# Kernel tuning notes

Hardware: AMD Instinct MI355X
Metric: run time of the kernel (lower is better)

Reference implementation:

```python
import jax, jax.numpy as jnp
import numpy as np

TAU = 1.0   # ltc_params['tau_constant']
DT = 0.1    # LTCCell default dt
UNFOLDS = 6 # ltc_params['ode_unfolds']
B, S, D, H, O = 512, 512, 128, 128, 1


def setup_inputs() -> dict:
    key = jax.random.key(0)
    ks = jax.random.split(key, 7)
    sc = lambda n: 1.0 / np.sqrt(n)
    return {
        "x":    jax.random.normal(ks[0], (B, S, D), dtype=jnp.float32),
        "W_in": jax.random.normal(ks[1], (H, D), dtype=jnp.float32) * sc(D),
        "b_in": jax.random.normal(ks[2], (H,), dtype=jnp.float32) * sc(D),
        "W_r":  jax.random.normal(ks[3], (H, H), dtype=jnp.float32) * sc(H),
        "b_r":  jax.random.normal(ks[4], (H,), dtype=jnp.float32) * sc(H),
        "W_fc": jax.random.normal(ks[5], (O, H), dtype=jnp.float32) * sc(H),
        "b_fc": jax.random.normal(ks[6], (O,), dtype=jnp.float32) * sc(H),
    }


def reference(x, W_in, b_in, W_r, b_r, W_fc, b_fc):
    # input_map(x[:, t]) is invariant across the inner unfold loop -> precompute once.
    xin_all = jnp.einsum('bsd,hd->bsh', x, W_in) + b_in  # [B,S,H]

    def step(h, xin):  # h: [B,H], xin: [B,H]
        for _ in range(UNFOLDS):  # small fixed count, unrolled
            v = jnp.tanh(xin + h @ W_r.T + b_r)
            h = h + DT * (-h / TAU + v)
        return h, None

    h0 = jnp.zeros((x.shape[0], W_r.shape[0]), dtype=x.dtype)
    h, _ = jax.lax.scan(step, h0, jnp.swapaxes(xin_all, 0, 1))  # scan over seq
    return (h @ W_fc.T + b_fc).squeeze(-1)  # [B]
```

## Files before the change

### kernel.cpp

```cpp
#include <hip/hip_runtime.h>


typedef _Float16 v2h __attribute__((ext_vector_type(2)));

#define S_LEN 512
#define HDIM 128
#define BATCH 512
#define NUNF 6
#define DTC 0.1f

__device__ __forceinline__ v2h pk2h(float a, float b) {
    return __builtin_bit_cast(v2h, __builtin_amdgcn_cvt_pkrtz(a, b));
}

__device__ __forceinline__ float fast_tanh(float y) {
    float u = __expf(2.0f * y);
    return 1.0f - __fdividef(2.0f, u + 1.0f);
}

__global__ __launch_bounds__(256, 2)
void xin_kernel(const float* __restrict__ x,
                const float* __restrict__ W_in,
                const float* __restrict__ b_in,
                unsigned int* __restrict__ xin)
{
    __shared__ __align__(16) _Float16 xt[128 * HDIM];
    const int tid  = threadIdx.x;
    const int w    = tid >> 6;
    const int lane = tid & 63;
    const int bs0  = blockIdx.x * 128;

    const float4* xg = reinterpret_cast<const float4*>(x + (size_t)bs0 * HDIM);
#pragma unroll
    for (int i = 0; i < 16; ++i) {
        int idx = i * 1024 + tid * 4;
        float4 v = xg[idx >> 2];
        v2h* d = reinterpret_cast<v2h*>(xt + idx);
        d[0] = pk2h(v.x, v.y);
        d[1] = pk2h(v.z, v.w);
    }

    v2h wi0[64], wi1[64];
    {
        const float4* r0 = reinterpret_cast<const float4*>(W_in + (size_t)lane * HDIM);
        const float4* r1 = reinterpret_cast<const float4*>(W_in + (size_t)(lane + 64) * HDIM);
#pragma unroll
        for (int j = 0; j < 32; ++j) {
            float4 f = r0[j];
            wi0[2*j]   = pk2h(f.x, f.y);
            wi0[2*j+1] = pk2h(f.z, f.w);
            float4 g = r1[j];
            wi1[2*j]   = pk2h(g.x, g.y);
            wi1[2*j+1] = pk2h(g.z, g.w);
        }
    }
    const float bi0 = b_in[lane], bi1 = b_in[lane + 64];
    __syncthreads();

    for (int rr = 0; rr < 32; ++rr) {
        const int r = w * 32 + rr;
        const float4* hp = reinterpret_cast<const float4*>(xt + r * HDIM);
        float a0 = 0.f, a1 = 0.f, c0 = 0.f, c1 = 0.f;
#pragma unroll
        for (int j = 0; j < 16; ++j) {
            float4 q = hp[j];
            const v2h* hh = reinterpret_cast<const v2h*>(&q);
            a0 = __builtin_amdgcn_fdot2(wi0[4*j+0], hh[0], a0, false);
            a1 = __builtin_amdgcn_fdot2(wi0[4*j+1], hh[1], a1, false);
            a0 = __builtin_amdgcn_fdot2(wi0[4*j+2], hh[2], a0, false);
            a1 = __builtin_amdgcn_fdot2(wi0[4*j+3], hh[3], a1, false);
            c0 = __builtin_amdgcn_fdot2(wi1[4*j+0], hh[0], c0, false);
            c1 = __builtin_amdgcn_fdot2(wi1[4*j+1], hh[1], c1, false);
            c0 = __builtin_amdgcn_fdot2(wi1[4*j+2], hh[2], c0, false);
            c1 = __builtin_amdgcn_fdot2(wi1[4*j+3], hh[3], c1, false);
        }
        v2h pk = pk2h(a0 + a1 + bi0, c0 + c1 + bi1);
        xin[(size_t)(bs0 + r) * 64 + lane] = __builtin_bit_cast(unsigned int, pk);
    }
}

__global__ __launch_bounds__(64, 1)
void ltc_kernel(const unsigned int* __restrict__ xin,
                const float* __restrict__ W_r,
                const float* __restrict__ b_r,
                const float* __restrict__ W_fc,
                const float* __restrict__ b_fc,
                float* __restrict__ out)
{
    const int b  = blockIdx.x;
    const int ln = threadIdx.x;
    const int o0 = ln, o1 = ln + 64;

    __shared__ __align__(16) v2h hbuf[64];

    v2h wr0[64], wr1[64];
    {
        const float4* lo0 = reinterpret_cast<const float4*>(W_r + (size_t)o0 * HDIM);
        const float4* hi0 = reinterpret_cast<const float4*>(W_r + (size_t)o0 * HDIM + 64);
        const float4* lo1 = reinterpret_cast<const float4*>(W_r + (size_t)o1 * HDIM);
        const float4* hi1 = reinterpret_cast<const float4*>(W_r + (size_t)o1 * HDIM + 64);
#pragma unroll
        for (int j = 0; j < 16; ++j) {
            float4 a = lo0[j], h = hi0[j];
            wr0[4*j+0] = pk2h(a.x, h.x);
            wr0[4*j+1] = pk2h(a.y, h.y);
            wr0[4*j+2] = pk2h(a.z, h.z);
            wr0[4*j+3] = pk2h(a.w, h.w);
            float4 c = lo1[j], d = hi1[j];
            wr1[4*j+0] = pk2h(c.x, d.x);
            wr1[4*j+1] = pk2h(c.y, d.y);
            wr1[4*j+2] = pk2h(c.z, d.z);
            wr1[4*j+3] = pk2h(c.w, d.w);
        }
    }
    const float br0 = b_r[o0], br1 = b_r[o1];
    const unsigned int* xrow = xin + (size_t)b * S_LEN * 64;

    float h0 = 0.f, h1 = 0.f;
    hbuf[ln] = v2h{(_Float16)0.f, (_Float16)0.f};
    unsigned int xcur = xrow[ln];

    for (int s = 0; s < S_LEN; ++s) {
        unsigned int xnext = 0;
        if (s + 1 < S_LEN) xnext = xrow[(s + 1) * 64 + ln];
        v2h xp = __builtin_bit_cast(v2h, xcur);
        const float xs0 = (float)xp.x + br0;
        const float xs1 = (float)xp.y + br1;

#pragma unroll
        for (int u = 0; u < NUNF; ++u) {
            const float4* hp = reinterpret_cast<const float4*>(hbuf);
            float a0 = 0.f, a1 = 0.f, c0 = 0.f, c1 = 0.f;
#pragma unroll
            for (int j = 0; j < 16; ++j) {
                float4 q = hp[j];
                const v2h* hh = reinterpret_cast<const v2h*>(&q);
                a0 = __builtin_amdgcn_fdot2(wr0[4*j+0], hh[0], a0, false);
                a1 = __builtin_amdgcn_fdot2(wr0[4*j+1], hh[1], a1, false);
                a0 = __builtin_amdgcn_fdot2(wr0[4*j+2], hh[2], a0, false);
                a1 = __builtin_amdgcn_fdot2(wr0[4*j+3], hh[3], a1, false);
                c0 = __builtin_amdgcn_fdot2(wr1[4*j+0], hh[0], c0, false);
                c1 = __builtin_amdgcn_fdot2(wr1[4*j+1], hh[1], c1, false);
                c0 = __builtin_amdgcn_fdot2(wr1[4*j+2], hh[2], c0, false);
                c1 = __builtin_amdgcn_fdot2(wr1[4*j+3], hh[3], c1, false);
            }
            float v0 = fast_tanh(xs0 + a0 + a1);
            float v1 = fast_tanh(xs1 + c0 + c1);
            h0 = h0 + DTC * (v0 - h0);
            h1 = h1 + DTC * (v1 - h1);
            hbuf[ln] = pk2h(h0, h1);
        }
        xcur = xnext;
    }

    float partial = h0 * W_fc[o0] + h1 * W_fc[o1];
#pragma unroll
    for (int d = 1; d < 64; d <<= 1) partial += __shfl_xor(partial, d);
    if (ln == 0) out[b] = partial + b_fc[0];
}

__global__ __launch_bounds__(256, 2)
void ltc_fallback(const float* __restrict__ x,
                  const float* __restrict__ W_in,
                  const float* __restrict__ b_in,
                  const float* __restrict__ W_r,
                  const float* __restrict__ b_r,
                  const float* __restrict__ W_fc,
                  const float* __restrict__ b_fc,
                  float* __restrict__ out)
{
    const int b     = blockIdx.x;
    const int tid   = threadIdx.x;
    const int o     = tid >> 1;
    const int kh    = tid & 1;
    const int kbase = kh * 64;

    __shared__ __align__(16) _Float16 hbuf[2][HDIM];
    __shared__ __align__(16) _Float16 xbuf[2][HDIM];
    __shared__ float red[4];

    v2h wr[32], wi[32];
    {
        const float4* wrp = reinterpret_cast<const float4*>(W_r  + o * HDIM + kbase);
        const float4* wip = reinterpret_cast<const float4*>(W_in + o * HDIM + kbase);
#pragma unroll
        for (int j = 0; j < 16; ++j) {
            float4 f = wrp[j];
            wr[2*j]   = pk2h(f.x, f.y);
            wr[2*j+1] = pk2h(f.z, f.w);
            float4 g = wip[j];
            wi[2*j]   = pk2h(g.x, g.y);
            wi[2*j+1] = pk2h(g.z, g.w);
        }
    }
    const float binv = b_in[o];
    const float brv  = b_r[o];
    const float* x_row = x + (size_t)b * S_LEN * HDIM;
    float h_o = 0.0f;

    if (tid < HDIM) {
        xbuf[0][tid] = (_Float16)x_row[tid];
        hbuf[0][tid] = (_Float16)0.0f;
    }
    __syncthreads();

    for (int s = 0; s < S_LEN; ++s) {
        float xnext = 0.0f;
        if (tid < HDIM && s + 1 < S_LEN)
            xnext = x_row[(size_t)(s + 1) * HDIM + tid];

        float xin_o;
        {
            const float4* hp = reinterpret_cast<const float4*>(&xbuf[s & 1][kbase]);
            float4 hv[8];
#pragma unroll
            for (int j = 0; j < 8; ++j) hv[j] = hp[j];
            const v2h* hh = reinterpret_cast<const v2h*>(hv);
            float a0 = 0.f, a1 = 0.f, a2 = 0.f, a3 = 0.f;
#pragma unroll
            for (int j = 0; j < 32; j += 4) {
                a0 = __builtin_amdgcn_fdot2(wi[j],   hh[j],   a0, false);
                a1 = __builtin_amdgcn_fdot2(wi[j+1], hh[j+1], a1, false);
                a2 = __builtin_amdgcn_fdot2(wi[j+2], hh[j+2], a2, false);
                a3 = __builtin_amdgcn_fdot2(wi[j+3], hh[j+3], a3, false);
            }
            float sum = (a0 + a1) + (a2 + a3);
            sum += __shfl_xor(sum, 1);
            xin_o = sum + binv;
        }

#pragma unroll
        for (int u = 0; u < NUNF; ++u) {
            const float4* hp = reinterpret_cast<const float4*>(&hbuf[u & 1][kbase]);
            float4 hv[8];
#pragma unroll
            for (int j = 0; j < 8; ++j) hv[j] = hp[j];
            const v2h* hh = reinterpret_cast<const v2h*>(hv);
            float a0 = 0.f, a1 = 0.f, a2 = 0.f, a3 = 0.f;
#pragma unroll
            for (int j = 0; j < 32; j += 4) {
                a0 = __builtin_amdgcn_fdot2(wr[j],   hh[j],   a0, false);
                a1 = __builtin_amdgcn_fdot2(wr[j+1], hh[j+1], a1, false);
                a2 = __builtin_amdgcn_fdot2(wr[j+2], hh[j+2], a2, false);
                a3 = __builtin_amdgcn_fdot2(wr[j+3], hh[j+3], a3, false);
            }
            float sum = (a0 + a1) + (a2 + a3);
            sum += __shfl_xor(sum, 1);
            float yv = xin_o + brv + sum;
            float v  = fast_tanh(yv);
            h_o = h_o + DTC * (v - h_o);
            if ((tid & 1) == 0)
                hbuf[(u + 1) & 1][o] = (_Float16)h_o;
            if (u == NUNF - 1 && tid < HDIM && s + 1 < S_LEN)
                xbuf[(s + 1) & 1][tid] = (_Float16)xnext;
            __syncthreads();
        }
    }

    float partial = 0.0f;
    if ((tid & 1) == 0) partial = h_o * W_fc[o];
#pragma unroll
    for (int d = 1; d < 64; d <<= 1) partial += __shfl_xor(partial, d);
    if ((tid & 63) == 0) red[tid >> 6] = partial;
    __syncthreads();
    if (tid == 0) out[b] = red[0] + red[1] + red[2] + red[3] + b_fc[0];
}

extern "C" void kernel_launch(void* const* d_in, const int* in_sizes, int n_in,
                              void* d_out, int out_size, void* d_ws, size_t ws_size,
                              hipStream_t stream) {
    const float* x    = (const float*)d_in[0];
    const float* W_in = (const float*)d_in[1];
    const float* b_in = (const float*)d_in[2];
    const float* W_r  = (const float*)d_in[3];
    const float* b_r  = (const float*)d_in[4];
    const float* W_fc = (const float*)d_in[5];
    const float* b_fc = (const float*)d_in[6];
    float* outp = (float*)d_out;
    (void)in_sizes; (void)n_in; (void)out_size;

    const size_t need = (size_t)BATCH * S_LEN * 64 * sizeof(unsigned int);
    if (ws_size >= need) {
        unsigned int* xin = (unsigned int*)d_ws;
        xin_kernel<<<dim3(2048), dim3(256), 0, stream>>>(x, W_in, b_in, xin);
        ltc_kernel<<<dim3(512), dim3(64), 0, stream>>>(xin, W_r, b_r, W_fc, b_fc, outp);
    } else {
        ltc_fallback<<<dim3(512), dim3(256), 0, stream>>>(x, W_in, b_in, W_r, b_r, W_fc, b_fc, outp);
    }
}
```

Before: 1.620 ms.

## Split recurrent step across two wavefronts, one output neuron per thread

Moves the recurrent kernel from one 64-lane wavefront handling two hidden units per lane to a 128-thread block where each thread owns one hidden unit. This halves the per-thread dot-product chain and the register-held weights. In exchange it needs a block-wide barrier after every unfold, uses double-buffered shared hidden state, and adds a cross-wave reduction at the end. The serial recurrence is latency-bound, so the gain depends on whether the shorter dependency chain outweighs the barrier cost.

```diff
diff --git a/kernel.cpp b/kernel.cpp
--- a/kernel.cpp
+++ b/kernel.cpp
@@ -79,7 +79,7 @@
     }
 }
 
-__global__ __launch_bounds__(64, 1)
+__global__ __launch_bounds__(128, 1)
 void ltc_kernel(const unsigned int* __restrict__ xin,
                 const float* __restrict__ W_r,
                 const float* __restrict__ b_r,
@@ -87,76 +87,66 @@
                 const float* __restrict__ b_fc,
                 float* __restrict__ out)
 {
-    const int b  = blockIdx.x;
-    const int ln = threadIdx.x;
-    const int o0 = ln, o1 = ln + 64;
-
-    __shared__ __align__(16) v2h hbuf[64];
-
-    v2h wr0[64], wr1[64];
+    const int b   = blockIdx.x;
+    const int tid = threadIdx.x;
+    const int w   = tid >> 6;
+    const int ln  = tid & 63;
+    const int od  = tid;
+
+    __shared__ __align__(16) _Float16 hbuf[2][HDIM];
+    __shared__ float red[2];
+
+    v2h wr[64];
     {
-        const float4* lo0 = reinterpret_cast<const float4*>(W_r + (size_t)o0 * HDIM);
-        const float4* hi0 = reinterpret_cast<const float4*>(W_r + (size_t)o0 * HDIM + 64);
-        const float4* lo1 = reinterpret_cast<const float4*>(W_r + (size_t)o1 * HDIM);
-        const float4* hi1 = reinterpret_cast<const float4*>(W_r + (size_t)o1 * HDIM + 64);
-#pragma unroll
-        for (int j = 0; j < 16; ++j) {
-            float4 a = lo0[j], h = hi0[j];
-            wr0[4*j+0] = pk2h(a.x, h.x);
-            wr0[4*j+1] = pk2h(a.y, h.y);
-            wr0[4*j+2] = pk2h(a.z, h.z);
-            wr0[4*j+3] = pk2h(a.w, h.w);
-            float4 c = lo1[j], d = hi1[j];
-            wr1[4*j+0] = pk2h(c.x, d.x);
-            wr1[4*j+1] = pk2h(c.y, d.y);
-            wr1[4*j+2] = pk2h(c.z, d.z);
-            wr1[4*j+3] = pk2h(c.w, d.w);
-        }
-    }
-    const float br0 = b_r[o0], br1 = b_r[o1];
+        const float4* wp = reinterpret_cast<const float4*>(W_r + (size_t)od * HDIM);
+#pragma unroll
+        for (int j = 0; j < 32; ++j) {
+            float4 f = wp[j];
+            wr[2*j]   = pk2h(f.x, f.y);
+            wr[2*j+1] = pk2h(f.z, f.w);
+        }
+    }
+    const float brv = b_r[od];
     const unsigned int* xrow = xin + (size_t)b * S_LEN * 64;
 
-    float h0 = 0.f, h1 = 0.f;
-    hbuf[ln] = v2h{(_Float16)0.f, (_Float16)0.f};
+    float h = 0.f;
+    hbuf[0][tid] = (_Float16)0.f;
+    __syncthreads();
+
     unsigned int xcur = xrow[ln];
-
     for (int s = 0; s < S_LEN; ++s) {
         unsigned int xnext = 0;
         if (s + 1 < S_LEN) xnext = xrow[(s + 1) * 64 + ln];
         v2h xp = __builtin_bit_cast(v2h, xcur);
-        const float xs0 = (float)xp.x + br0;
-        const float xs1 = (float)xp.y + br1;
+        const float xs = (w ? (float)xp.y : (float)xp.x) + brv;
 
 #pragma unroll
         for (int u = 0; u < NUNF; ++u) {
-            const float4* hp = reinterpret_cast<const float4*>(hbuf);
-            float a0 = 0.f, a1 = 0.f, c0 = 0.f, c1 = 0.f;
+            const float4* hp = reinterpret_cast<const float4*>(hbuf[u & 1]);
+            float a0 = 0.f, a1 = 0.f, a2 = 0.f, a3 = 0.f;
 #pragma unroll
             for (int j = 0; j < 16; ++j) {
                 float4 q = hp[j];
                 const v2h* hh = reinterpret_cast<const v2h*>(&q);
-                a0 = __builtin_amdgcn_fdot2(wr0[4*j+0], hh[0], a0, false);
-                a1 = __builtin_amdgcn_fdot2(wr0[4*j+1], hh[1], a1, false);
-                a0 = __builtin_amdgcn_fdot2(wr0[4*j+2], hh[2], a0, false);
-                a1 = __builtin_amdgcn_fdot2(wr0[4*j+3], hh[3], a1, false);
-                c0 = __builtin_amdgcn_fdot2(wr1[4*j+0], hh[0], c0, false);
-                c1 = __builtin_amdgcn_fdot2(wr1[4*j+1], hh[1], c1, false);
-                c0 = __builtin_amdgcn_fdot2(wr1[4*j+2], hh[2], c0, false);
-                c1 = __builtin_amdgcn_fdot2(wr1[4*j+3], hh[3], c1, false);
+                a0 = __builtin_amdgcn_fdot2(wr[4*j+0], hh[0], a0, false);
+                a1 = __builtin_amdgcn_fdot2(wr[4*j+1], hh[1], a1, false);
+                a2 = __builtin_amdgcn_fdot2(wr[4*j+2], hh[2], a2, false);
+                a3 = __builtin_amdgcn_fdot2(wr[4*j+3], hh[3], a3, false);
             }
-            float v0 = fast_tanh(xs0 + a0 + a1);
-            float v1 = fast_tanh(xs1 + c0 + c1);
-            h0 = h0 + DTC * (v0 - h0);
-            h1 = h1 + DTC * (v1 - h1);
-            hbuf[ln] = pk2h(h0, h1);
+            float v = fast_tanh(xs + (a0 + a1) + (a2 + a3));
+            h = h + DTC * (v - h);
+            hbuf[(u + 1) & 1][od] = (_Float16)h;
+            __syncthreads();
         }
         xcur = xnext;
     }
 
-    float partial = h0 * W_fc[o0] + h1 * W_fc[o1];
+    float partial = h * W_fc[od];
 #pragma unroll
     for (int d = 1; d < 64; d <<= 1) partial += __shfl_xor(partial, d);
-    if (ln == 0) out[b] = partial + b_fc[0];
+    if (ln == 0) red[w] = partial;
+    __syncthreads();
+    if (tid == 0) out[b] = red[0] + red[1] + b_fc[0];
 }
 
 __global__ __launch_bounds__(256, 2)
@@ -283,7 +273,7 @@
     if (ws_size >= need) {
         unsigned int* xin = (unsigned int*)d_ws;
         xin_kernel<<<dim3(2048), dim3(256), 0, stream>>>(x, W_in, b_in, xin);
-        ltc_kernel<<<dim3(512), dim3(64), 0, stream>>>(xin, W_r, b_r, W_fc, b_fc, outp);
+        ltc_kernel<<<dim3(512), dim3(128), 0, stream>>>(xin, W_r, b_r, W_fc, b_fc, outp);
     } else {
         ltc_fallback<<<dim3(512), dim3(256), 0, stream>>>(x, W_in, b_in, W_r, b_r, W_fc, b_fc, outp);
     }
```

Result: slower. 1.673 ms (+3.3%).
